# Kernel optimization log

Measured on AMD Instinct MI355X. Metric: run time of the kernel, lower is better.

## Reference

```python
import jax, jax.numpy as jnp
import numpy as np
from jax import lax

B, T, BYTE_LEN, EMB = 8, 4096, 8, 64
FILTERS = [(1, 4), (2, 8), (3, 12), (4, 16), (5, 20), (6, 24), (7, 28)]
LAST_DIM = sum(c for _, c in FILTERS)  # 112
OUT_DIM = 512


def setup_inputs() -> dict:
    key = jax.random.key(0)
    ks = jax.random.split(key, 32)
    inp = {"features": jax.random.normal(ks[0], (B, T, BYTE_LEN, EMB), dtype=jnp.float32)}
    for i, (w, c) in enumerate(FILTERS):
        inp[f"conv_w{i+1}"] = jax.random.normal(ks[1 + i], (c, EMB, w), dtype=jnp.float32) * 0.05
        inp[f"conv_b{i+1}"] = jax.random.normal(ks[8 + i], (c,), dtype=jnp.float32) * 0.05
    inp["hw_w1"] = jax.random.normal(ks[15], (2 * LAST_DIM, LAST_DIM), dtype=jnp.float32) * 0.05
    inp["hw_b1"] = jnp.concatenate([jnp.zeros(LAST_DIM), jnp.ones(LAST_DIM)]).astype(jnp.float32)
    inp["hw_w2"] = jax.random.normal(ks[16], (2 * LAST_DIM, LAST_DIM), dtype=jnp.float32) * 0.05
    inp["hw_b2"] = jnp.concatenate([jnp.zeros(LAST_DIM), jnp.ones(LAST_DIM)]).astype(jnp.float32)
    inp["proj_w"] = jax.random.normal(ks[17], (OUT_DIM, LAST_DIM), dtype=jnp.float32) * 0.05
    inp["proj_b"] = jax.random.normal(ks[18], (OUT_DIM,), dtype=jnp.float32) * 0.05
    return inp


def _conv_branch(x, w, b):
    # x: [N, EMB, BYTE_LEN], w: [out_c, EMB, width] -> max over time, relu -> [N, out_c]
    y = lax.conv_general_dilated(x, w, window_strides=(1,), padding='VALID',
                                 dimension_numbers=('NCH', 'OIH', 'NCH'))
    y = y + b[None, :, None]
    return jax.nn.relu(jnp.max(y, axis=-1))


def _highway_layer(x, w, b):
    p = x @ w.T + b
    proj_x, gate = jnp.split(p, 2, axis=-1)
    g = jax.nn.sigmoid(gate)
    return g * x + (1.0 - g) * jax.nn.relu(proj_x)


def reference(features, conv_w1, conv_w2, conv_w3, conv_w4, conv_w5, conv_w6, conv_w7,
              conv_b1, conv_b2, conv_b3, conv_b4, conv_b5, conv_b6, conv_b7,
              hw_w1, hw_b1, hw_w2, hw_b2, proj_w, proj_b):
    b, t, byte_len, emb = features.shape
    # transpose(2,3).view(-1, emb, byte_len)
    x = features.transpose(0, 1, 3, 2).reshape(-1, emb, byte_len)  # [B*T, EMB, BYTE_LEN]
    ws = [conv_w1, conv_w2, conv_w3, conv_w4, conv_w5, conv_w6, conv_w7]
    bs = [conv_b1, conv_b2, conv_b3, conv_b4, conv_b5, conv_b6, conv_b7]
    branches = [_conv_branch(x, w, bb) for w, bb in zip(ws, bs)]
    h = jnp.concatenate(branches, axis=-1)  # [B*T, LAST_DIM]
    h = _highway_layer(h, hw_w1, hw_b1)
    h = _highway_layer(h, hw_w2, hw_b2)
    out = h @ proj_w.T + proj_b  # [B*T, OUT_DIM]
    return out.reshape(b, t, -1)
```

## Files before the change

### kernel.cpp

```cpp
#include <hip/hip_runtime.h>

typedef __attribute__((ext_vector_type(8))) short short8;
typedef __attribute__((ext_vector_type(4))) float f32x4;

#define NPOS 32768
#define KDIM 512
#define NCT  30
#define CHUNK_BYTES 30720

__device__ __forceinline__ unsigned short f2bf(float x) {
    unsigned u = __float_as_uint(x);
    return (unsigned short)((u + 0x7FFFu + ((u >> 16) & 1u)) >> 16);
}
__device__ __forceinline__ float bf2f(unsigned short h) {
    return __uint_as_float(((unsigned)h) << 16);
}

__device__ __forceinline__ void stage16(const void* g, void* l, int lane) {
    __builtin_amdgcn_global_load_lds(
        (const __attribute__((address_space(1))) unsigned int*)g,
        (__attribute__((address_space(3))) unsigned int*)l, 16, 0, 0);
}

__global__ void prep_kernel(const float* __restrict__ w1, const float* __restrict__ w2,
                            const float* __restrict__ w3, const float* __restrict__ w4,
                            const float* __restrict__ w5, const float* __restrict__ w6,
                            const float* __restrict__ w7, const float* __restrict__ hw1,
                            const float* __restrict__ hw2, const float* __restrict__ pw,
                            unsigned short* __restrict__ WC, unsigned short* __restrict__ W1s,
                            unsigned short* __restrict__ W2s, unsigned short* __restrict__ Ps) {
    int gid = blockIdx.x * 256 + threadIdx.x;
    if (gid < 245760) {
        int k = gid / 480, col = gid % 480;
        const float* wp; int cbnd, NP, C, W;
        if (col < 32)       { wp = w1; cbnd = 0;   NP = 8; C = 4;  W = 1; }
        else if (col < 96)  { wp = w2; cbnd = 32;  NP = 7; C = 8;  W = 2; }
        else if (col < 176) { wp = w3; cbnd = 96;  NP = 6; C = 12; W = 3; }
        else if (col < 256) { wp = w4; cbnd = 176; NP = 5; C = 16; W = 4; }
        else if (col < 336) { wp = w5; cbnd = 256; NP = 4; C = 20; W = 5; }
        else if (col < 416) { wp = w6; cbnd = 336; NP = 3; C = 24; W = 6; }
        else                { wp = w7; cbnd = 416; NP = 2; C = 28; W = 7; }
        int c2 = col - cbnd, oc = c2 / NP, p = c2 - oc * NP;
        int j = k >> 6, e = k & 63, dk = j - p;
        float v = 0.f;
        if (oc < C && dk >= 0 && dk < W) v = wp[(oc * 64 + e) * W + dk];
        int q = k >> 5, kr = k & 31;
        WC[((q * NCT + (col >> 4)) * 64 + ((kr >> 3) * 16 + (col & 15))) * 8 + (kr & 7)] = f2bf(v);
    } else if (gid < 245760 + 57344) {
        int x = gid - 245760;
        const float* src = (x < 28672) ? hw1 : hw2;
        unsigned short* dst = (x < 28672) ? W1s : W2s;
        if (x >= 28672) x -= 28672;
        int k = x / 224, n = x % 224;
        float v = (k < 112) ? src[n * 112 + k] : 0.f;
        int q = k >> 5, kr = k & 31;
        dst[((q * 14 + (n >> 4)) * 64 + ((kr >> 3) * 16 + (n & 15))) * 8 + (kr & 7)] = f2bf(v);
    } else if (gid < 245760 + 57344 + 65536) {
        int x = gid - 303104;
        int k = x / 512, n = x % 512;
        float v = (k < 112) ? pw[n * 112 + k] : 0.f;
        int q = k >> 5, kr = k & 31;
        Ps[((q * 32 + (n >> 4)) * 64 + ((kr >> 3) * 16 + (n & 15))) * 8 + (kr & 7)] = f2bf(v);
    }
}

template <int T0, int NT>
__device__ __forceinline__ void dump_phase(float* Cb, const f32x4* acc, int wave, int lane) {
    int r0 = wave * 16 + ((lane >> 4) * 4);
    int c0 = lane & 15;
#pragma unroll
    for (int tt = 0; tt < NT; ++tt)
#pragma unroll
        for (int r = 0; r < 4; ++r)
            Cb[(r0 + r) * 161 + tt * 16 + c0] = acc[T0 + tt][r];
}

__device__ void reduce_phase(const float* Cb, unsigned short* ht, int tid,
                             int cA, int NPA, int choffA, int colbA, const float* cbA,
                             int cB, int NPB, int choffB, int colbB, const float* cbB) {
    int noc = cA + cB;
    for (int idx = tid; idx < 64 * noc; idx += 256) {
        int row = idx & 63, ocp = idx >> 6;
        bool isB = ocp >= cA;
        int oc = isB ? ocp - cA : ocp;
        int NP = isB ? NPB : NPA;
        int colb = isB ? colbB : colbA;
        int choff = isB ? choffB : choffA;
        const float* cb = isB ? cbB : cbA;
        const float* src = Cb + row * 161 + colb + oc * NP;
        float m = src[0];
        for (int k = 1; k < NP; ++k) m = fmaxf(m, src[k]);
        float v = fmaxf(m + cb[oc], 0.f);
        ht[row * 128 + choff + oc] = f2bf(v);
    }
}

__global__ __launch_bounds__(256, 2) void conv_gemm(
        const float* __restrict__ feat, const unsigned short* __restrict__ WC,
        const float* cb0, const float* cb1, const float* cb2, const float* cb3,
        const float* cb4, const float* cb5, const float* cb6,
        unsigned short* __restrict__ hg) {
    __shared__ __align__(16) char sm[61440];
    const int tid = threadIdx.x, lane = tid & 63, wave = tid >> 6;
    const int c0 = lane & 15, kq = lane >> 4;
    const int m0 = blockIdx.x * 64;

    const float* arow = feat + (size_t)(m0 + wave * 16 + c0) * KDIM + kq * 8;
    short8 af[16];
#pragma unroll
    for (int q = 0; q < 16; ++q) {
        float t[8];
        *(float4*)(t)     = *(const float4*)(arow + q * 32);
        *(float4*)(t + 4) = *(const float4*)(arow + q * 32 + 4);
        short8 v;
#pragma unroll
        for (int i = 0; i < 8; ++i) v[i] = (short)f2bf(t[i]);
        af[q] = v;
    }

    f32x4 zero = {0.f, 0.f, 0.f, 0.f};
    f32x4 acc[NCT];
#pragma unroll
    for (int t = 0; t < NCT; ++t) acc[t] = zero;

    for (int i = tid; i < 1920; i += 256)
        stage16(WC + i * 8, sm + (i - lane) * 16, lane);

#pragma unroll
    for (int q = 0; q < 16; ++q) {
        __syncthreads();
        if (q < 15) {
            const unsigned short* src = WC + (q + 1) * (CHUNK_BYTES / 2);
            char* dst = sm + ((q + 1) & 1) * CHUNK_BYTES;
            for (int i = tid; i < 1920; i += 256)
                stage16(src + i * 8, dst + (i - lane) * 16, lane);
        }
        const char* bb = sm + (q & 1) * CHUNK_BYTES;
#pragma unroll
        for (int t = 0; t < NCT; ++t) {
            short8 b = *(const short8*)(bb + (t * 64 + lane) * 16);
            acc[t] = __builtin_amdgcn_mfma_f32_16x16x32_bf16(af[q], b, acc[t], 0, 0, 0);
        }
    }

    float* Cb = (float*)sm;
    unsigned short* ht = (unsigned short*)(sm + 41216);
    __syncthreads();
    for (int i = tid; i < 1024; i += 256)
        ht[(i >> 4) * 128 + 112 + (i & 15)] = 0;
    dump_phase<0, 6>(Cb, acc, wave, lane);
    __syncthreads();
    reduce_phase(Cb, ht, tid, 4, 8, 0, 0, cb0, 8, 7, 4, 32, cb1);
    __syncthreads();
    dump_phase<6, 10>(Cb, acc, wave, lane);
    __syncthreads();
    reduce_phase(Cb, ht, tid, 12, 6, 12, 0, cb2, 16, 5, 24, 80, cb3);
    __syncthreads();
    dump_phase<16, 10>(Cb, acc, wave, lane);
    __syncthreads();
    reduce_phase(Cb, ht, tid, 20, 4, 40, 0, cb4, 24, 3, 60, 80, cb5);
    __syncthreads();
    dump_phase<26, 4>(Cb, acc, wave, lane);
    __syncthreads();
    reduce_phase(Cb, ht, tid, 28, 2, 84, 0, cb6, 0, 1, 0, 0, cb6);
    __syncthreads();
    uint4* dst = (uint4*)(hg + (size_t)m0 * 128);
    for (int i = tid; i < 1024; i += 256) dst[i] = ((const uint4*)ht)[i];
}

__global__ __launch_bounds__(256, 2) void tail_kernel(
        const unsigned short* __restrict__ hg, const unsigned short* __restrict__ W1,
        const unsigned short* __restrict__ W2, const unsigned short* __restrict__ PW,
        const float* __restrict__ hb1, const float* __restrict__ hb2,
        const float* __restrict__ pb, float* __restrict__ out) {
    __shared__ __align__(16) char sm[65536];
    const int tid = threadIdx.x, lane = tid & 63, wave = tid >> 6;
    const int c0 = lane & 15, kq = lane >> 4;
    const int m0 = blockIdx.x * 64;
    f32x4 zero = {0.f, 0.f, 0.f, 0.f};

    short8 a2[4];
#pragma unroll
    for (int q = 0; q < 4; ++q)
        a2[q] = *(const short8*)(hg + (size_t)(m0 + wave * 16 + c0) * 128 + q * 32 + kq * 8);

    for (int i = tid; i < 3584; i += 256)
        stage16(W1 + i * 8, sm + (i - lane) * 16, lane);
    __syncthreads();
    f32x4 acc2[14];
#pragma unroll
    for (int t = 0; t < 14; ++t) acc2[t] = zero;
#pragma unroll
    for (int t = 0; t < 14; ++t)
#pragma unroll
        for (int q = 0; q < 4; ++q) {
            short8 b = *(const short8*)(sm + ((q * 14 + t) * 64 + lane) * 16);
            acc2[t] = __builtin_amdgcn_mfma_f32_16x16x32_bf16(a2[q], b, acc2[t], 0, 0, 0);
        }
    __syncthreads();

    unsigned short* ht = (unsigned short*)sm;
#pragma unroll
    for (int t = 0; t < 7; ++t) {
        float bp = hb1[t * 16 + c0], bg = hb1[112 + t * 16 + c0];
#pragma unroll
        for (int r = 0; r < 4; ++r) {
            int row = wave * 16 + kq * 4 + r;
            int col = t * 16 + c0;
            float px = acc2[t][r] + bp;
            float gt = acc2[t + 7][r] + bg;
            float g = 1.f / (1.f + __expf(-gt));
            float hres = bf2f(hg[(size_t)(m0 + row) * 128 + col]);
            ht[row * 136 + col] = f2bf(g * hres + (1.f - g) * fmaxf(px, 0.f));
        }
    }
    for (int z = lane; z < 256; z += 64)
        ht[(wave * 16 + (z >> 4)) * 136 + 112 + (z & 15)] = 0;

    short8 a3[4];
#pragma unroll
    for (int q = 0; q < 4; ++q)
        a3[q] = *(const short8*)((const char*)ht + (wave * 16 + c0) * 272 + q * 64 + kq * 16);

    char* wbuf = sm + 17408;
    f32x4 acc3[14];
#pragma unroll
    for (int t = 0; t < 14; ++t) acc3[t] = zero;
    for (int i = tid; i < 1792; i += 256)
        stage16(W2 + i * 8, wbuf + (i - lane) * 16, lane);
    __syncthreads();
#pragma unroll
    for (int t = 0; t < 14; ++t)
#pragma unroll
        for (int q = 0; q < 2; ++q) {
            short8 b = *(const short8*)(wbuf + ((q * 14 + t) * 64 + lane) * 16);
            acc3[t] = __builtin_amdgcn_mfma_f32_16x16x32_bf16(a3[q], b, acc3[t], 0, 0, 0);
        }
    __syncthreads();
    for (int i = tid; i < 1792; i += 256)
        stage16(W2 + 14336 + i * 8, wbuf + (i - lane) * 16, lane);
    __syncthreads();
#pragma unroll
    for (int t = 0; t < 14; ++t)
#pragma unroll
        for (int q = 0; q < 2; ++q) {
            short8 b = *(const short8*)(wbuf + ((q * 14 + t) * 64 + lane) * 16);
            acc3[t] = __builtin_amdgcn_mfma_f32_16x16x32_bf16(a3[2 + q], b, acc3[t], 0, 0, 0);
        }

#pragma unroll
    for (int t = 0; t < 7; ++t) {
        float bp = hb2[t * 16 + c0], bg = hb2[112 + t * 16 + c0];
#pragma unroll
        for (int r = 0; r < 4; ++r) {
            int row = wave * 16 + kq * 4 + r;
            int col = t * 16 + c0;
            float px = acc3[t][r] + bp;
            float gt = acc3[t + 7][r] + bg;
            float g = 1.f / (1.f + __expf(-gt));
            float hres = bf2f(ht[row * 136 + col]);
            ht[row * 136 + col] = f2bf(g * hres + (1.f - g) * fmaxf(px, 0.f));
        }
    }

    short8 a4[4];
#pragma unroll
    for (int q = 0; q < 4; ++q)
        a4[q] = *(const short8*)((const char*)ht + (wave * 16 + c0) * 272 + q * 64 + kq * 16);

    f32x4 acc4[32];
#pragma unroll
    for (int t = 0; t < 32; ++t) acc4[t] = zero;
#pragma unroll
    for (int q = 0; q < 4; ++q) {
        __syncthreads();
        for (int i = tid; i < 2048; i += 256)
            stage16(PW + q * 16384 + i * 8, wbuf + (i - lane) * 16, lane);
        __syncthreads();
#pragma unroll
        for (int t = 0; t < 32; ++t) {
            short8 b = *(const short8*)(wbuf + (t * 64 + lane) * 16);
            acc4[t] = __builtin_amdgcn_mfma_f32_16x16x32_bf16(a4[q], b, acc4[t], 0, 0, 0);
        }
    }

    float* ot = (float*)sm;
#pragma unroll
    for (int half = 0; half < 2; ++half) {
        __syncthreads();
#pragma unroll
        for (int t16 = 0; t16 < 16; ++t16) {
            int col = (half * 16 + t16) * 16 + c0;
            float b = pb[col];
#pragma unroll
            for (int r = 0; r < 4; ++r)
                ot[(wave * 16 + kq * 4 + r) * 256 + t16 * 16 + c0] = acc4[half * 16 + t16][r] + b;
        }
        __syncthreads();
        for (int i = tid; i < 4096; i += 256) {
            int row = i >> 6, c = i & 63;
            *(float4*)(out + (size_t)(m0 + row) * 512 + half * 256 + c * 4) = ((const float4*)ot)[i];
        }
    }
}

extern "C" void kernel_launch(void* const* d_in, const int* in_sizes, int n_in,
                              void* d_out, int out_size, void* d_ws, size_t ws_size,
                              hipStream_t stream) {
    const float* feat = (const float*)d_in[0];
    const float* cw[7];
    const float* cb[7];
    for (int f = 0; f < 7; ++f) {
        cw[f] = (const float*)d_in[1 + 2 * f];
        cb[f] = (const float*)d_in[2 + 2 * f];
    }
    const float* hw_w1 = (const float*)d_in[15];
    const float* hw_b1 = (const float*)d_in[16];
    const float* hw_w2 = (const float*)d_in[17];
    const float* hw_b2 = (const float*)d_in[18];
    const float* pw    = (const float*)d_in[19];
    const float* pb    = (const float*)d_in[20];
    float* out = (float*)d_out;

    char* ws = (char*)d_ws;
    unsigned short* WC  = (unsigned short*)ws;
    unsigned short* W1s = (unsigned short*)(ws + 491520);
    unsigned short* W2s = (unsigned short*)(ws + 548864);
    unsigned short* Ps  = (unsigned short*)(ws + 606208);
    unsigned short* hg  = (unsigned short*)(ws + 737280);

    prep_kernel<<<1440, 256, 0, stream>>>(cw[0], cw[1], cw[2], cw[3], cw[4], cw[5], cw[6],
                                          hw_w1, hw_w2, pw, WC, W1s, W2s, Ps);
    conv_gemm<<<512, 256, 0, stream>>>(feat, WC, cb[0], cb[1], cb[2], cb[3], cb[4], cb[5], cb[6], hg);
    tail_kernel<<<512, 256, 0, stream>>>(hg, W1s, W2s, Ps, hw_b1, hw_b2, pb, out);
}
```

Measured before the change: 200.9 us.

## Fuse conv GEMM and highway/projection tail into one kernel with pipelined weight staging

Merges the conv GEMM kernel and the tail kernel into a single kernel, so the conv output tile stays in shared memory (stride 136) instead of making a round trip through global memory. This drops one launch and the global write and read of the intermediate. The highway and projection weight loads are restaged as double-buffered chunks that overlap with the MFMA work, where before they were loaded as blocking bulk transfers. The cost is a longer fused kernel whose register pressure (the conv and projection accumulators) may hurt occupancy or cause spills.

Result: faster. 192.8 us (-4.0%).

```diff
diff --git a/kernel.cpp b/kernel.cpp
--- a/kernel.cpp
+++ b/kernel.cpp
@@ -91,86 +91,16 @@
         float m = src[0];
         for (int k = 1; k < NP; ++k) m = fmaxf(m, src[k]);
         float v = fmaxf(m + cb[oc], 0.f);
-        ht[row * 128 + choff + oc] = f2bf(v);
-    }
-}
-
-__global__ __launch_bounds__(256, 2) void conv_gemm(
+        ht[row * 136 + choff + oc] = f2bf(v);
+    }
+}
+
+__global__ __launch_bounds__(256, 2) void fused_kernel(
         const float* __restrict__ feat, const unsigned short* __restrict__ WC,
         const float* cb0, const float* cb1, const float* cb2, const float* cb3,
         const float* cb4, const float* cb5, const float* cb6,
-        unsigned short* __restrict__ hg) {
-    __shared__ __align__(16) char sm[61440];
-    const int tid = threadIdx.x, lane = tid & 63, wave = tid >> 6;
-    const int c0 = lane & 15, kq = lane >> 4;
-    const int m0 = blockIdx.x * 64;
-
-    const float* arow = feat + (size_t)(m0 + wave * 16 + c0) * KDIM + kq * 8;
-    short8 af[16];
-#pragma unroll
-    for (int q = 0; q < 16; ++q) {
-        float t[8];
-        *(float4*)(t)     = *(const float4*)(arow + q * 32);
-        *(float4*)(t + 4) = *(const float4*)(arow + q * 32 + 4);
-        short8 v;
-#pragma unroll
-        for (int i = 0; i < 8; ++i) v[i] = (short)f2bf(t[i]);
-        af[q] = v;
-    }
-
-    f32x4 zero = {0.f, 0.f, 0.f, 0.f};
-    f32x4 acc[NCT];
-#pragma unroll
-    for (int t = 0; t < NCT; ++t) acc[t] = zero;
-
-    for (int i = tid; i < 1920; i += 256)
-        stage16(WC + i * 8, sm + (i - lane) * 16, lane);
-
-#pragma unroll
-    for (int q = 0; q < 16; ++q) {
-        __syncthreads();
-        if (q < 15) {
-            const unsigned short* src = WC + (q + 1) * (CHUNK_BYTES / 2);
-            char* dst = sm + ((q + 1) & 1) * CHUNK_BYTES;
-            for (int i = tid; i < 1920; i += 256)
-                stage16(src + i * 8, dst + (i - lane) * 16, lane);
-        }
-        const char* bb = sm + (q & 1) * CHUNK_BYTES;
-#pragma unroll
-        for (int t = 0; t < NCT; ++t) {
-            short8 b = *(const short8*)(bb + (t * 64 + lane) * 16);
-            acc[t] = __builtin_amdgcn_mfma_f32_16x16x32_bf16(af[q], b, acc[t], 0, 0, 0);
-        }
-    }
-
-    float* Cb = (float*)sm;
-    unsigned short* ht = (unsigned short*)(sm + 41216);
-    __syncthreads();
-    for (int i = tid; i < 1024; i += 256)
-        ht[(i >> 4) * 128 + 112 + (i & 15)] = 0;
-    dump_phase<0, 6>(Cb, acc, wave, lane);
-    __syncthreads();
-    reduce_phase(Cb, ht, tid, 4, 8, 0, 0, cb0, 8, 7, 4, 32, cb1);
-    __syncthreads();
-    dump_phase<6, 10>(Cb, acc, wave, lane);
-    __syncthreads();
-    reduce_phase(Cb, ht, tid, 12, 6, 12, 0, cb2, 16, 5, 24, 80, cb3);
-    __syncthreads();
-    dump_phase<16, 10>(Cb, acc, wave, lane);
-    __syncthreads();
-    reduce_phase(Cb, ht, tid, 20, 4, 40, 0, cb4, 24, 3, 60, 80, cb5);
-    __syncthreads();
-    dump_phase<26, 4>(Cb, acc, wave, lane);
-    __syncthreads();
-    reduce_phase(Cb, ht, tid, 28, 2, 84, 0, cb6, 0, 1, 0, 0, cb6);
-    __syncthreads();
-    uint4* dst = (uint4*)(hg + (size_t)m0 * 128);
-    for (int i = tid; i < 1024; i += 256) dst[i] = ((const uint4*)ht)[i];
-}
-
-__global__ __launch_bounds__(256, 2) void tail_kernel(
-        const unsigned short* __restrict__ hg, const unsigned short* __restrict__ W1,
-        const unsigned short* __restrict__ W2, const unsigned short* __restrict__ PW,
+        const unsigned short* __restrict__ W1, const unsigned short* __restrict__ W2,
+        const unsigned short* __restrict__ PW,
         const float* __restrict__ hb1, const float* __restrict__ hb2,
         const float* __restrict__ pb, float* __restrict__ out) {
     __shared__ __align__(16) char sm[65536];
@@ -179,27 +109,96 @@
     const int m0 = blockIdx.x * 64;
     f32x4 zero = {0.f, 0.f, 0.f, 0.f};
 
+    const float* arow = feat + (size_t)(m0 + wave * 16 + c0) * KDIM + kq * 8;
+    short8 af[16];
+#pragma unroll
+    for (int q = 0; q < 16; ++q) {
+        float t[8];
+        *(float4*)(t)     = *(const float4*)(arow + q * 32);
+        *(float4*)(t + 4) = *(const float4*)(arow + q * 32 + 4);
+        short8 v;
+#pragma unroll
+        for (int i = 0; i < 8; ++i) v[i] = (short)f2bf(t[i]);
+        af[q] = v;
+    }
+
+    f32x4 acc[NCT];
+#pragma unroll
+    for (int t = 0; t < NCT; ++t) acc[t] = zero;
+
+    for (int i = tid; i < 1920; i += 256)
+        stage16(WC + i * 8, sm + (i - lane) * 16, lane);
+
+#pragma unroll
+    for (int q = 0; q < 16; ++q) {
+        __syncthreads();
+        if (q < 15) {
+            const unsigned short* src = WC + (q + 1) * (CHUNK_BYTES / 2);
+            char* dst = sm + ((q + 1) & 1) * CHUNK_BYTES;
+            for (int i = tid; i < 1920; i += 256)
+                stage16(src + i * 8, dst + (i - lane) * 16, lane);
+        }
+        const char* bb = sm + (q & 1) * CHUNK_BYTES;
+#pragma unroll
+        for (int t = 0; t < NCT; ++t) {
+            short8 b = *(const short8*)(bb + (t * 64 + lane) * 16);
+            acc[t] = __builtin_amdgcn_mfma_f32_16x16x32_bf16(af[q], b, acc[t], 0, 0, 0);
+        }
+    }
+
+    float* Cb = (float*)sm;
+    unsigned short* ht = (unsigned short*)(sm + 41216);
+    __syncthreads();
+    for (int i = tid; i < 1024; i += 256)
+        ht[(i >> 4) * 136 + 112 + (i & 15)] = 0;
+    dump_phase<0, 6>(Cb, acc, wave, lane);
+    __syncthreads();
+    reduce_phase(Cb, ht, tid, 4, 8, 0, 0, cb0, 8, 7, 4, 32, cb1);
+    __syncthreads();
+    dump_phase<6, 10>(Cb, acc, wave, lane);
+    __syncthreads();
+    reduce_phase(Cb, ht, tid, 12, 6, 12, 0, cb2, 16, 5, 24, 80, cb3);
+    __syncthreads();
+    dump_phase<16, 10>(Cb, acc, wave, lane);
+    __syncthreads();
+    reduce_phase(Cb, ht, tid, 20, 4, 40, 0, cb4, 24, 3, 60, 80, cb5);
+    __syncthreads();
+    dump_phase<26, 4>(Cb, acc, wave, lane);
+    __syncthreads();
+    reduce_phase(Cb, ht, tid, 28, 2, 84, 0, cb6, 0, 1, 0, 0, cb6);
+    __syncthreads();
+
+    char* wb = sm;
     short8 a2[4];
 #pragma unroll
     for (int q = 0; q < 4; ++q)
-        a2[q] = *(const short8*)(hg + (size_t)(m0 + wave * 16 + c0) * 128 + q * 32 + kq * 8);
-
-    for (int i = tid; i < 3584; i += 256)
-        stage16(W1 + i * 8, sm + (i - lane) * 16, lane);
-    __syncthreads();
+        a2[q] = *(const short8*)((const char*)ht + (wave * 16 + c0) * 272 + q * 64 + kq * 16);
+    for (int i = tid; i < 896; i += 256)
+        stage16(W1 + i * 8, wb + (i - lane) * 16, lane);
+
     f32x4 acc2[14];
 #pragma unroll
     for (int t = 0; t < 14; ++t) acc2[t] = zero;
 #pragma unroll
-    for (int t = 0; t < 14; ++t)
-#pragma unroll
-        for (int q = 0; q < 4; ++q) {
-            short8 b = *(const short8*)(sm + ((q * 14 + t) * 64 + lane) * 16);
+    for (int q = 0; q < 4; ++q) {
+        __syncthreads();
+        if (q < 3) {
+            const unsigned short* src = W1 + (q + 1) * 7168;
+            char* dst = wb + ((q + 1) & 1) * 14336;
+            for (int i = tid; i < 896; i += 256)
+                stage16(src + i * 8, dst + (i - lane) * 16, lane);
+        }
+        const char* bb = wb + (q & 1) * 14336;
+#pragma unroll
+        for (int t = 0; t < 14; ++t) {
+            short8 b = *(const short8*)(bb + (t * 64 + lane) * 16);
             acc2[t] = __builtin_amdgcn_mfma_f32_16x16x32_bf16(a2[q], b, acc2[t], 0, 0, 0);
         }
-    __syncthreads();
-
-    unsigned short* ht = (unsigned short*)sm;
+    }
+
+    for (int i = tid; i < 896; i += 256)
+        stage16(W2 + i * 8, wb + (i - lane) * 16, lane);
+
 #pragma unroll
     for (int t = 0; t < 7; ++t) {
         float bp = hb1[t * 16 + c0], bg = hb1[112 + t * 16 + c0];
@@ -210,43 +209,36 @@
             float px = acc2[t][r] + bp;
             float gt = acc2[t + 7][r] + bg;
             float g = 1.f / (1.f + __expf(-gt));
-            float hres = bf2f(hg[(size_t)(m0 + row) * 128 + col]);
+            float hres = bf2f(ht[row * 136 + col]);
             ht[row * 136 + col] = f2bf(g * hres + (1.f - g) * fmaxf(px, 0.f));
         }
     }
-    for (int z = lane; z < 256; z += 64)
-        ht[(wave * 16 + (z >> 4)) * 136 + 112 + (z & 15)] = 0;
+    __syncthreads();
 
     short8 a3[4];
 #pragma unroll
     for (int q = 0; q < 4; ++q)
         a3[q] = *(const short8*)((const char*)ht + (wave * 16 + c0) * 272 + q * 64 + kq * 16);
 
-    char* wbuf = sm + 17408;
     f32x4 acc3[14];
 #pragma unroll
     for (int t = 0; t < 14; ++t) acc3[t] = zero;
-    for (int i = tid; i < 1792; i += 256)
-        stage16(W2 + i * 8, wbuf + (i - lane) * 16, lane);
-    __syncthreads();
-#pragma unroll
-    for (int t = 0; t < 14; ++t)
-#pragma unroll
-        for (int q = 0; q < 2; ++q) {
-            short8 b = *(const short8*)(wbuf + ((q * 14 + t) * 64 + lane) * 16);
+#pragma unroll
+    for (int q = 0; q < 4; ++q) {
+        __syncthreads();
+        if (q < 3) {
+            const unsigned short* src = W2 + (q + 1) * 7168;
+            char* dst = wb + ((q + 1) & 1) * 14336;
+            for (int i = tid; i < 896; i += 256)
+                stage16(src + i * 8, dst + (i - lane) * 16, lane);
+        }
+        const char* bb = wb + (q & 1) * 14336;
+#pragma unroll
+        for (int t = 0; t < 14; ++t) {
+            short8 b = *(const short8*)(bb + (t * 64 + lane) * 16);
             acc3[t] = __builtin_amdgcn_mfma_f32_16x16x32_bf16(a3[q], b, acc3[t], 0, 0, 0);
         }
-    __syncthreads();
-    for (int i = tid; i < 1792; i += 256)
-        stage16(W2 + 14336 + i * 8, wbuf + (i - lane) * 16, lane);
-    __syncthreads();
-#pragma unroll
-    for (int t = 0; t < 14; ++t)
-#pragma unroll
-        for (int q = 0; q < 2; ++q) {
-            short8 b = *(const short8*)(wbuf + ((q * 14 + t) * 64 + lane) * 16);
-            acc3[t] = __builtin_amdgcn_mfma_f32_16x16x32_bf16(a3[2 + q], b, acc3[t], 0, 0, 0);
-        }
+    }
 
 #pragma unroll
     for (int t = 0; t < 7; ++t) {
@@ -262,25 +254,35 @@
             ht[row * 136 + col] = f2bf(g * hres + (1.f - g) * fmaxf(px, 0.f));
         }
     }
+    __syncthreads();
 
     short8 a4[4];
 #pragma unroll
     for (int q = 0; q < 4; ++q)
         a4[q] = *(const short8*)((const char*)ht + (wave * 16 + c0) * 272 + q * 64 + kq * 16);
 
+    char* pwb = sm;
+    for (int i = tid; i < 1024; i += 256)
+        stage16(PW + i * 8, pwb + (i - lane) * 16, lane);
+
     f32x4 acc4[32];
 #pragma unroll
     for (int t = 0; t < 32; ++t) acc4[t] = zero;
 #pragma unroll
-    for (int q = 0; q < 4; ++q) {
-        __syncthreads();
-        for (int i = tid; i < 2048; i += 256)
-            stage16(PW + q * 16384 + i * 8, wbuf + (i - lane) * 16, lane);
-        __syncthreads();
-#pragma unroll
-        for (int t = 0; t < 32; ++t) {
-            short8 b = *(const short8*)(wbuf + (t * 64 + lane) * 16);
-            acc4[t] = __builtin_amdgcn_mfma_f32_16x16x32_bf16(a4[q], b, acc4[t], 0, 0, 0);
+    for (int c = 0; c < 8; ++c) {
+        __syncthreads();
+        if (c < 7) {
+            const unsigned short* src = PW + (c + 1) * 8192;
+            char* dst = pwb + ((c + 1) & 1) * 16384;
+            for (int i = tid; i < 1024; i += 256)
+                stage16(src + i * 8, dst + (i - lane) * 16, lane);
+        }
+        const char* bb = pwb + (c & 1) * 16384;
+#pragma unroll
+        for (int tt = 0; tt < 16; ++tt) {
+            short8 b = *(const short8*)(bb + (tt * 64 + lane) * 16);
+            acc4[(c & 1) * 16 + tt] =
+                __builtin_amdgcn_mfma_f32_16x16x32_bf16(a4[c >> 1], b, acc4[(c & 1) * 16 + tt], 0, 0, 0);
         }
     }
 
@@ -327,10 +329,9 @@
     unsigned short* W1s = (unsigned short*)(ws + 491520);
     unsigned short* W2s = (unsigned short*)(ws + 548864);
     unsigned short* Ps  = (unsigned short*)(ws + 606208);
-    unsigned short* hg  = (unsigned short*)(ws + 737280);
 
     prep_kernel<<<1440, 256, 0, stream>>>(cw[0], cw[1], cw[2], cw[3], cw[4], cw[5], cw[6],
                                           hw_w1, hw_w2, pw, WC, W1s, W2s, Ps);
-    conv_gemm<<<512, 256, 0, stream>>>(feat, WC, cb[0], cb[1], cb[2], cb[3], cb[4], cb[5], cb[6], hg);
-    tail_kernel<<<512, 256, 0, stream>>>(hg, W1s, W2s, Ps, hw_b1, hw_b2, pb, out);
-}
+    fused_kernel<<<512, 256, 0, stream>>>(feat, WC, cb[0], cb[1], cb[2], cb[3], cb[4], cb[5], cb[6],
+                                          W1s, W2s, Ps, hw_b1, hw_b2, pb, out);
+}
```
